# Performance work log

Measured on AMD Instinct MI355X. Metric: run time of the kernel, lower is better.

Reference implementation:

```python
import jax, jax.numpy as jnp
import numpy as np

B, DIM, N = 4, 256, 2048
HEADS, DIM_HEAD = 8, 64
HIDDEN = HEADS * DIM_HEAD
SCALE = DIM_HEAD ** -0.5


def setup_inputs() -> dict:
    key = jax.random.key(0)
    k0, k1, k2, k3 = jax.random.split(key, 4)
    x = jax.random.normal(k0, (B, DIM, N), dtype=jnp.float32)
    # Conv1d kernel-size-1 weights == plain matrices over channels
    w_qkv = jax.random.normal(k1, (3 * HIDDEN, DIM), dtype=jnp.float32) * (DIM ** -0.5)
    w_out = jax.random.normal(k2, (DIM, HIDDEN), dtype=jnp.float32) * (HIDDEN ** -0.5)
    b_out = jax.random.normal(k3, (DIM,), dtype=jnp.float32) * 0.01
    return {"x": x, "w_qkv": w_qkv, "w_out": w_out, "b_out": b_out}


def reference(x, w_qkv, w_out, b_out):
    b, c, n = x.shape
    # 1x1 conv projection: [3H, C] x [b, C, n] -> [b, 3H, n]
    qkv = jnp.einsum('oc,bcn->bon', w_qkv, x)
    q, k, v = jnp.split(qkv, 3, axis=1)
    # [b, heads, dim_head, n]
    q = q.reshape(b, HEADS, DIM_HEAD, n) * SCALE
    k = k.reshape(b, HEADS, DIM_HEAD, n)
    v = v.reshape(b, HEADS, DIM_HEAD, n)
    sim = jnp.einsum('bhcn,bhcm->bhnm', q, k)          # [b,h,n,n]
    attn = jax.nn.softmax(sim, axis=-1)
    out = jnp.einsum('bhnm,bhcm->bhcn', attn, v)       # [b,h,dh,n]
    out = out.reshape(b, HIDDEN, n)
    return jnp.einsum('oc,bcn->bon', w_out, out) + b_out[None, :, None]
```

## Files before the change

kernel.cpp:

```cpp
#include <hip/hip_runtime.h>
#include <math.h>

#define BB 4
#define CDIM 256
#define NN 2048
#define HEADS 8
#define DH 64
#define HIDDEN 512
#define THREEH 1536
#define QSCALE 0.18033688011112042f

typedef __attribute__((ext_vector_type(8))) short bf16x8;
typedef __attribute__((ext_vector_type(4))) float f32x4;

static __device__ inline unsigned short f2bf(float f) {
    unsigned u = __float_as_uint(f);
    u += 0x7fff + ((u >> 16) & 1);
    return (unsigned short)(u >> 16);
}
#if __has_builtin(__builtin_amdgcn_cvt_pk_bf16_f32)
static __device__ inline unsigned pk2(float a, float b) {
    auto v = __builtin_amdgcn_cvt_pk_bf16_f32(a, b);
    return __builtin_bit_cast(unsigned, v);
}
#else
static __device__ inline unsigned pk2(float a, float b) {
    return (unsigned)f2bf(a) | ((unsigned)f2bf(b) << 16);
}
#endif
#if __has_builtin(__builtin_amdgcn_exp2f)
#define EXP2(x) __builtin_amdgcn_exp2f(x)
#else
#define EXP2(x) exp2f(x)
#endif
#define MFMA16(a, b, c) __builtin_amdgcn_mfma_f32_16x16x32_bf16(a, b, c, 0, 0, 0)
#define SWZC(row, ch) ((((ch) ^ ((row) & 7)) << 3))

__global__ __launch_bounds__(256) void prep_w(const float* __restrict__ wqkv,
                                              const float* __restrict__ wout,
                                              unsigned* __restrict__ Wqb,
                                              unsigned* __restrict__ Wob) {
    const int t = blockIdx.x * 256 + threadIdx.x;
    if (t < 98304) {
        const int e = t * 4;
        const int o = e >> 8;
        const float s = (o < HIDDEN) ? QSCALE : 1.f;
        float4 v = *(const float4*)&wqkv[e];
        Wqb[t * 2 + 0] = pk2(v.x * s, v.y * s);
        Wqb[t * 2 + 1] = pk2(v.z * s, v.w * s);
    } else {
        const int e = (t - 98304) * 4;
        float4 v = *(const float4*)&wout[e];
        Wob[(t - 98304) * 2 + 0] = pk2(v.x, v.y);
        Wob[(t - 98304) * 2 + 1] = pk2(v.z, v.w);
    }
}

__global__ __launch_bounds__(256) void prep_x(const float* __restrict__ x,
                                              unsigned short* __restrict__ Xt) {
    __shared__ float Ls[64][65];
    const int n0 = blockIdx.x * 64, c0 = blockIdx.y * 64, b = blockIdx.z;
    const int t = threadIdx.x;
    const int r16 = t >> 4, c16 = t & 15;
#pragma unroll
    for (int s = 0; s < 4; ++s) {
        const int c = s * 16 + r16;
        float4 v = *(const float4*)&x[((size_t)(b * CDIM + c0 + c)) * NN + n0 + c16 * 4];
        *(float4*)&Ls[c][c16 * 4] = v;
    }
    __syncthreads();
#pragma unroll
    for (int s = 0; s < 4; ++s) {
        const int n = s * 16 + r16;
        const int c4 = c16 * 4;
        uint2 u;
        u.x = pk2(Ls[c4][n], Ls[c4 + 1][n]);
        u.y = pk2(Ls[c4 + 2][n], Ls[c4 + 3][n]);
        *(uint2*)&Xt[((size_t)(b * NN) + n0 + n) * CDIM + c0 + c4] = u;
    }
}

__global__ __launch_bounds__(256, 3) void qkv_gemm(const unsigned short* __restrict__ Xt,
                                                   const unsigned short* __restrict__ Wqb,
                                                   unsigned short* __restrict__ Qb,
                                                   unsigned short* __restrict__ Kb,
                                                   unsigned short* __restrict__ Vb) {
    __shared__ unsigned short Xs[128 * 64], Ws[128 * 64];
    const int bn0 = blockIdx.x * 128, o0 = blockIdx.y * 128;
    const int t = threadIdx.x, l = t & 63, w = t >> 6, lo = l & 15, quad = l >> 4;
    const int wo = (w >> 1) * 64, wn = (w & 1) * 64;
    const int sr = t >> 1, scb = (t & 1) * 4;
    const bool isV = (o0 >= 2 * HIDDEN);
    f32x4 acc[4][4];
#pragma unroll
    for (int i = 0; i < 4; ++i)
#pragma unroll
        for (int j = 0; j < 4; ++j) acc[i][j] = (f32x4){0.f, 0.f, 0.f, 0.f};

    for (int kc = 0; kc < CDIM; kc += 64) {
        __syncthreads();
#pragma unroll
        for (int j = 0; j < 4; ++j) {
            const int ch = scb + j;
            *(uint4*)&Xs[sr * 64 + SWZC(sr, ch)] =
                *(const uint4*)&Xt[(size_t)(bn0 + sr) * CDIM + kc + ch * 8];
            *(uint4*)&Ws[sr * 64 + SWZC(sr, ch)] =
                *(const uint4*)&Wqb[(size_t)(o0 + sr) * CDIM + kc + ch * 8];
        }
        __syncthreads();
#pragma unroll
        for (int kk = 0; kk < 2; ++kk) {
            const int swz = SWZC(lo, kk * 4 + quad);
            if (!isV) {
                bf16x8 af[4], bv[4];
#pragma unroll
                for (int ot = 0; ot < 4; ++ot) af[ot] = *(const bf16x8*)&Ws[(wo + ot * 16 + lo) * 64 + swz];
#pragma unroll
                for (int nt = 0; nt < 4; ++nt) bv[nt] = *(const bf16x8*)&Xs[(wn + nt * 16 + lo) * 64 + swz];
#pragma unroll
                for (int ot = 0; ot < 4; ++ot)
#pragma unroll
                    for (int nt = 0; nt < 4; ++nt) acc[ot][nt] = MFMA16(af[ot], bv[nt], acc[ot][nt]);
            } else {
                bf16x8 af[4], bv[4];
#pragma unroll
                for (int mt = 0; mt < 4; ++mt) af[mt] = *(const bf16x8*)&Xs[(wn + mt * 16 + lo) * 64 + swz];
#pragma unroll
                for (int ot = 0; ot < 4; ++ot) bv[ot] = *(const bf16x8*)&Ws[(wo + ot * 16 + lo) * 64 + swz];
#pragma unroll
                for (int mt = 0; mt < 4; ++mt)
#pragma unroll
                    for (int ot = 0; ot < 4; ++ot) acc[mt][ot] = MFMA16(af[mt], bv[ot], acc[mt][ot]);
            }
        }
    }
    if (!isV) {
#pragma unroll
        for (int ot = 0; ot < 4; ++ot) {
            const int og = o0 + wo + ot * 16 + quad * 4;
            const int h = (og >> 6) & 7;
            const int c0 = og & 63;
            unsigned short* dst = (og >= HIDDEN) ? Kb : Qb;
#pragma unroll
            for (int nt = 0; nt < 4; ++nt) {
                const int bn = bn0 + wn + nt * 16 + lo;
                const int b = bn >> 11, n = bn & 2047;
                uint2 u;
                u.x = pk2(acc[ot][nt][0], acc[ot][nt][1]);
                u.y = pk2(acc[ot][nt][2], acc[ot][nt][3]);
                *(uint2*)&dst[(((size_t)(b * HEADS + h)) * NN + n) * DH + c0] = u;
            }
        }
    } else {
#pragma unroll
        for (int mt = 0; mt < 4; ++mt) {
            const int bn = bn0 + wn + mt * 16 + quad * 4;
            const int b = bn >> 11, m = bn & 2047;
#pragma unroll
            for (int ot = 0; ot < 4; ++ot) {
                const int og = o0 + wo + ot * 16 + lo;
                const int h = (og >> 6) & 7;
                const int c = og & 63;
                uint2 u;
                u.x = pk2(acc[mt][ot][0], acc[mt][ot][1]);
                u.y = pk2(acc[mt][ot][2], acc[mt][ot][3]);
                *(uint2*)&Vb[(((size_t)(b * HEADS + h)) * DH + c) * NN + m] = u;
            }
        }
    }
}

__global__ __launch_bounds__(256, 6) void flash_attn(const unsigned short* __restrict__ Qb,
                                                     const unsigned short* __restrict__ Kb,
                                                     const unsigned short* __restrict__ Vb,
                                                     unsigned short* __restrict__ Yb) {
    __shared__ unsigned short Ks[64 * 64], Vs[64 * 64], Ps[64 * 64];
    const int flat = blockIdx.x;
    const int rest = flat >> 3;
    const int bh = ((rest & 3) << 3) | (flat & 7);
    const int q0 = (rest >> 2) * 64;
    const int b = bh >> 3, h = bh & 7;
    const int t = threadIdx.x, l = t & 63, w = t >> 6, lo = l & 15, quad = l >> 4;
    const unsigned short* Qp = Qb + (size_t)bh * NN * DH;
    const unsigned short* Kp = Kb + (size_t)bh * NN * DH;
    const unsigned short* Vp = Vb + (size_t)bh * DH * NN;
    const int q = q0 + 16 * w + lo;
    const bf16x8 bQ0 = *(const bf16x8*)&Qp[(size_t)q * DH + quad * 8];
    const bf16x8 bQ1 = *(const bf16x8*)&Qp[(size_t)q * DH + 32 + quad * 8];
    f32x4 O[4];
#pragma unroll
    for (int i = 0; i < 4; ++i) O[i] = (f32x4){0.f, 0.f, 0.f, 0.f};
    float m_i = -INFINITY, l_i = 0.f;
    const int sr = t >> 3, sc = t & 7;
    const int kst0 = sr * 64 + SWZC(sr, sc);
    const int key = lo & 7;

    for (int m0 = 0; m0 < NN; m0 += 64) {
        __syncthreads();
        *(uint4*)&Ks[kst0]           = *(const uint4*)&Kp[(size_t)(m0 + sr) * DH + sc * 8];
        *(uint4*)&Ks[kst0 + 32 * 64] = *(const uint4*)&Kp[(size_t)(m0 + sr + 32) * DH + sc * 8];
        *(uint4*)&Vs[kst0]           = *(const uint4*)&Vp[(size_t)sr * NN + m0 + sc * 8];
        *(uint4*)&Vs[kst0 + 32 * 64] = *(const uint4*)&Vp[(size_t)(sr + 32) * NN + m0 + sc * 8];
        __syncthreads();
        f32x4 S[4];
#pragma unroll
        for (int nt = 0; nt < 4; ++nt) {
            const int rb = (nt * 16 + lo) * 64;
            bf16x8 a0 = *(const bf16x8*)&Ks[rb + SWZC(lo, quad)];
            bf16x8 a1 = *(const bf16x8*)&Ks[rb + SWZC(lo, quad + 4)];
            f32x4 z = (f32x4){0.f, 0.f, 0.f, 0.f};
            z = MFMA16(a0, bQ0, z);
            z = MFMA16(a1, bQ1, z);
            S[nt] = z;
        }
        float mx;
        {
            f32x4 mm;
#pragma unroll
            for (int i = 0; i < 4; ++i)
                mm[i] = fmaxf(fmaxf(S[0][i], S[1][i]), fmaxf(S[2][i], S[3][i]));
            mx = fmaxf(fmaxf(mm[0], mm[1]), fmaxf(mm[2], mm[3]));
        }
        mx = fmaxf(mx, __shfl_xor(mx, 16));
        mx = fmaxf(mx, __shfl_xor(mx, 32));
        const float mn = fmaxf(m_i, mx);
        const float alpha = EXP2(m_i - mn);
        m_i = mn;
        float ls = 0.f;
        const int prow = (16 * w + lo) * 64;
#pragma unroll
        for (int nt = 0; nt < 4; ++nt) {
            f32x4 p;
#pragma unroll
            for (int i = 0; i < 4; ++i) p[i] = EXP2(S[nt][i] - mn);
            ls += (p[0] + p[1]) + (p[2] + p[3]);
            uint2 u;
            u.x = pk2(p[0], p[1]);
            u.y = pk2(p[2], p[3]);
            *(uint2*)&Ps[prow + (((nt * 2 + (quad >> 1)) ^ key) << 3) + (quad & 1) * 4] = u;
        }
        ls += __shfl_xor(ls, 16);
        ls += __shfl_xor(ls, 32);
        l_i = l_i * alpha + ls;
        asm volatile("s_waitcnt lgkmcnt(0)" ::: "memory");
#pragma unroll
        for (int ct = 0; ct < 4; ++ct) O[ct] *= alpha;
        const bf16x8 pb0 = *(const bf16x8*)&Ps[prow + SWZC(lo, quad)];
        const bf16x8 pb1 = *(const bf16x8*)&Ps[prow + SWZC(lo, quad + 4)];
#pragma unroll
        for (int ct = 0; ct < 4; ++ct) {
            const int rb = (ct * 16 + lo) * 64;
            bf16x8 a0 = *(const bf16x8*)&Vs[rb + SWZC(lo, quad)];
            bf16x8 a1 = *(const bf16x8*)&Vs[rb + SWZC(lo, quad + 4)];
            O[ct] = MFMA16(a0, pb0, O[ct]);
            O[ct] = MFMA16(a1, pb1, O[ct]);
        }
    }
    const float inv = 1.f / l_i;
    unsigned short* yrow = Yb + (((size_t)(b * NN) + q)) * HIDDEN + h * DH;
#pragma unroll
    for (int ct = 0; ct < 4; ++ct) {
        uint2 u;
        u.x = pk2(O[ct][0] * inv, O[ct][1] * inv);
        u.y = pk2(O[ct][2] * inv, O[ct][3] * inv);
        *(uint2*)&yrow[ct * 16 + quad * 4] = u;
    }
}

__global__ __launch_bounds__(256, 4) void out_gemm(const unsigned short* __restrict__ Yb,
                                                   const unsigned short* __restrict__ Wob,
                                                   const float* __restrict__ bias,
                                                   float* __restrict__ out) {
    __shared__ unsigned short Ys[128 * 64], Wos[64 * 64];
    const int bn0 = blockIdx.x * 128, o0 = blockIdx.y * 64;
    const int t = threadIdx.x, l = t & 63, w = t >> 6, lo = l & 15, quad = l >> 4;
    const int wn = w * 32;
    const int sr = t >> 1, scb = (t & 1) * 4;
    const int sr2 = t >> 2, scb2 = (t & 3) * 2;
    f32x4 acc[2][4];
#pragma unroll
    for (int i = 0; i < 2; ++i)
#pragma unroll
        for (int j = 0; j < 4; ++j) acc[i][j] = (f32x4){0.f, 0.f, 0.f, 0.f};

    for (int kc = 0; kc < HIDDEN; kc += 64) {
        __syncthreads();
#pragma unroll
        for (int j = 0; j < 4; ++j) {
            const int ch = scb + j;
            *(uint4*)&Ys[sr * 64 + SWZC(sr, ch)] =
                *(const uint4*)&Yb[(size_t)(bn0 + sr) * HIDDEN + kc + ch * 8];
        }
#pragma unroll
        for (int j = 0; j < 2; ++j) {
            const int ch = scb2 + j;
            *(uint4*)&Wos[sr2 * 64 + SWZC(sr2, ch)] =
                *(const uint4*)&Wob[(size_t)(o0 + sr2) * HIDDEN + kc + ch * 8];
        }
        __syncthreads();
#pragma unroll
        for (int kk = 0; kk < 2; ++kk) {
            const int swz = SWZC(lo, kk * 4 + quad);
            bf16x8 bv[4];
#pragma unroll
            for (int ot = 0; ot < 4; ++ot) bv[ot] = *(const bf16x8*)&Wos[(ot * 16 + lo) * 64 + swz];
#pragma unroll
            for (int mt = 0; mt < 2; ++mt) {
                bf16x8 av = *(const bf16x8*)&Ys[(wn + mt * 16 + lo) * 64 + swz];
#pragma unroll
                for (int ot = 0; ot < 4; ++ot) acc[mt][ot] = MFMA16(av, bv[ot], acc[mt][ot]);
            }
        }
    }
#pragma unroll
    for (int mt = 0; mt < 2; ++mt) {
        const int bn = bn0 + wn + mt * 16 + quad * 4;
        const int b = bn >> 11, n = bn & 2047;
#pragma unroll
        for (int ot = 0; ot < 4; ++ot) {
            const int o = o0 + ot * 16 + lo;
            *(f32x4*)&out[((size_t)(b * CDIM + o)) * NN + n] = acc[mt][ot] + bias[o];
        }
    }
}

extern "C" void kernel_launch(void* const* d_in, const int* in_sizes, int n_in,
                              void* d_out, int out_size, void* d_ws, size_t ws_size,
                              hipStream_t stream) {
    const float* x     = (const float*)d_in[0];
    const float* w_qkv = (const float*)d_in[1];
    const float* w_out = (const float*)d_in[2];
    const float* b_out = (const float*)d_in[3];
    float* out = (float*)d_out;

    unsigned short* Wqb = (unsigned short*)d_ws;
    unsigned short* Wob = Wqb + (size_t)THREEH * CDIM;
    unsigned short* Xt  = Wob + (size_t)CDIM * HIDDEN;
    unsigned short* Qb  = Xt + (size_t)BB * NN * CDIM;
    unsigned short* Kb  = Qb + (size_t)BB * HEADS * NN * DH;
    unsigned short* Vb  = Kb + (size_t)BB * HEADS * NN * DH;
    unsigned short* Yb  = Vb + (size_t)BB * HEADS * DH * NN;

    prep_w<<<512, 256, 0, stream>>>(w_qkv, w_out, (unsigned*)Wqb, (unsigned*)Wob);
    prep_x<<<dim3(NN / 64, CDIM / 64, BB), 256, 0, stream>>>(x, Xt);
    qkv_gemm<<<dim3(BB * NN / 128, THREEH / 128), 256, 0, stream>>>(Xt, Wqb, Qb, Kb, Vb);
    flash_attn<<<1024, 256, 0, stream>>>(Qb, Kb, Vb, Yb);
    out_gemm<<<dim3(BB * NN / 128, CDIM / 64), 256, 0, stream>>>(Yb, Wob, b_out, out);
}
```

Before: 164.7 us.

## Merge prep kernels and widen flash-attention tile to 128 queries with register prefetch

Merges the two preprocessing kernels into one launch, removing a kernel launch. In flash attention, each wave now handles 32 queries, so every K/V tile loaded into shared memory serves twice as many MFMAs. The next K/V tile is prefetched into registers to overlap global loads with compute. The row sum is computed with a ones-vector MFMA instead of shuffles, and O is rescaled only when a row max changes. In exchange the kernel uses more registers, its occupancy hint drops to 4, and the grid is halved to 512 blocks.

```diff
diff --git a/kernel.cpp b/kernel.cpp
--- a/kernel.cpp
+++ b/kernel.cpp
@@ -36,47 +36,55 @@
 #define MFMA16(a, b, c) __builtin_amdgcn_mfma_f32_16x16x32_bf16(a, b, c, 0, 0, 0)
 #define SWZC(row, ch) ((((ch) ^ ((row) & 7)) << 3))
 
-__global__ __launch_bounds__(256) void prep_w(const float* __restrict__ wqkv,
-                                              const float* __restrict__ wout,
-                                              unsigned* __restrict__ Wqb,
-                                              unsigned* __restrict__ Wob) {
-    const int t = blockIdx.x * 256 + threadIdx.x;
-    if (t < 98304) {
-        const int e = t * 4;
-        const int o = e >> 8;
-        const float s = (o < HIDDEN) ? QSCALE : 1.f;
-        float4 v = *(const float4*)&wqkv[e];
-        Wqb[t * 2 + 0] = pk2(v.x * s, v.y * s);
-        Wqb[t * 2 + 1] = pk2(v.z * s, v.w * s);
+__global__ __launch_bounds__(256) void prep_all(const float* __restrict__ x,
+                                                const float* __restrict__ wqkv,
+                                                const float* __restrict__ wout,
+                                                unsigned short* __restrict__ Xt,
+                                                unsigned* __restrict__ Wqb,
+                                                unsigned* __restrict__ Wob) {
+    __shared__ float Ls[64][65];
+    const int bx = blockIdx.x;
+    if (bx < 512) {
+        const int n0 = (bx & 31) * 64, c0 = ((bx >> 5) & 3) * 64, b = bx >> 7;
+        const int t = threadIdx.x;
+        const int r16 = t >> 4, c16 = t & 15;
+#pragma unroll
+        for (int s = 0; s < 4; ++s) {
+            const int c = s * 16 + r16;
+            float4 v = *(const float4*)&x[((size_t)(b * CDIM + c0 + c)) * NN + n0 + c16 * 4];
+            *(float4*)&Ls[c][c16 * 4] = v;
+        }
+        __syncthreads();
+#pragma unroll
+        for (int s = 0; s < 4; ++s) {
+            const int n = s * 16 + r16;
+            const int c4 = c16 * 4;
+            uint2 u;
+            u.x = pk2(Ls[c4][n], Ls[c4 + 1][n]);
+            u.y = pk2(Ls[c4 + 2][n], Ls[c4 + 3][n]);
+            *(uint2*)&Xt[((size_t)(b * NN) + n0 + n) * CDIM + c0 + c4] = u;
+        }
+    } else if (bx < 536) {
+        const int tt = (bx - 512) * 256 + threadIdx.x;
+#pragma unroll 4
+        for (int j = 0; j < 16; ++j) {
+            const int i4 = tt + j * 6144;
+            const int e = i4 * 4;
+            const float s = ((e >> 8) < HIDDEN) ? QSCALE : 1.f;
+            float4 v = *(const float4*)&wqkv[e];
+            Wqb[i4 * 2 + 0] = pk2(v.x * s, v.y * s);
+            Wqb[i4 * 2 + 1] = pk2(v.z * s, v.w * s);
+        }
     } else {
-        const int e = (t - 98304) * 4;
-        float4 v = *(const float4*)&wout[e];
-        Wob[(t - 98304) * 2 + 0] = pk2(v.x, v.y);
-        Wob[(t - 98304) * 2 + 1] = pk2(v.z, v.w);
-    }
-}
-
-__global__ __launch_bounds__(256) void prep_x(const float* __restrict__ x,
-                                              unsigned short* __restrict__ Xt) {
-    __shared__ float Ls[64][65];
-    const int n0 = blockIdx.x * 64, c0 = blockIdx.y * 64, b = blockIdx.z;
-    const int t = threadIdx.x;
-    const int r16 = t >> 4, c16 = t & 15;
-#pragma unroll
-    for (int s = 0; s < 4; ++s) {
-        const int c = s * 16 + r16;
-        float4 v = *(const float4*)&x[((size_t)(b * CDIM + c0 + c)) * NN + n0 + c16 * 4];
-        *(float4*)&Ls[c][c16 * 4] = v;
-    }
-    __syncthreads();
-#pragma unroll
-    for (int s = 0; s < 4; ++s) {
-        const int n = s * 16 + r16;
-        const int c4 = c16 * 4;
-        uint2 u;
-        u.x = pk2(Ls[c4][n], Ls[c4 + 1][n]);
-        u.y = pk2(Ls[c4 + 2][n], Ls[c4 + 3][n]);
-        *(uint2*)&Xt[((size_t)(b * NN) + n0 + n) * CDIM + c0 + c4] = u;
+        const int tt = (bx - 536) * 256 + threadIdx.x;
+#pragma unroll 4
+        for (int j = 0; j < 16; ++j) {
+            const int i4 = tt + j * 2048;
+            const int e = i4 * 4;
+            float4 v = *(const float4*)&wout[e];
+            Wob[i4 * 2 + 0] = pk2(v.x, v.y);
+            Wob[i4 * 2 + 1] = pk2(v.z, v.w);
+        }
     }
 }
 
@@ -170,100 +178,150 @@
     }
 }
 
-__global__ __launch_bounds__(256, 6) void flash_attn(const unsigned short* __restrict__ Qb,
+__global__ __launch_bounds__(256, 4) void flash_attn(const unsigned short* __restrict__ Qb,
                                                      const unsigned short* __restrict__ Kb,
                                                      const unsigned short* __restrict__ Vb,
                                                      unsigned short* __restrict__ Yb) {
-    __shared__ unsigned short Ks[64 * 64], Vs[64 * 64], Ps[64 * 64];
+    __shared__ unsigned short Ks[64 * 64], Vs[64 * 64], Ps[128 * 64];
     const int flat = blockIdx.x;
     const int rest = flat >> 3;
     const int bh = ((rest & 3) << 3) | (flat & 7);
-    const int q0 = (rest >> 2) * 64;
+    const int q0 = (rest >> 2) * 128;
     const int b = bh >> 3, h = bh & 7;
     const int t = threadIdx.x, l = t & 63, w = t >> 6, lo = l & 15, quad = l >> 4;
     const unsigned short* Qp = Qb + (size_t)bh * NN * DH;
     const unsigned short* Kp = Kb + (size_t)bh * NN * DH;
     const unsigned short* Vp = Vb + (size_t)bh * DH * NN;
-    const int q = q0 + 16 * w + lo;
-    const bf16x8 bQ0 = *(const bf16x8*)&Qp[(size_t)q * DH + quad * 8];
-    const bf16x8 bQ1 = *(const bf16x8*)&Qp[(size_t)q * DH + 32 + quad * 8];
-    f32x4 O[4];
-#pragma unroll
-    for (int i = 0; i < 4; ++i) O[i] = (f32x4){0.f, 0.f, 0.f, 0.f};
-    float m_i = -INFINITY, l_i = 0.f;
+    const int qbase = q0 + 32 * w;
+    bf16x8 bQ[2][2];
+#pragma unroll
+    for (int qt = 0; qt < 2; ++qt)
+#pragma unroll
+        for (int hh = 0; hh < 2; ++hh)
+            bQ[qt][hh] = *(const bf16x8*)&Qp[(size_t)(qbase + qt * 16 + lo) * DH + hh * 32 + quad * 8];
+    f32x4 O[4][2], lacc[2];
+#pragma unroll
+    for (int i = 0; i < 4; ++i)
+#pragma unroll
+        for (int j = 0; j < 2; ++j) O[i][j] = (f32x4){0.f, 0.f, 0.f, 0.f};
+#pragma unroll
+    for (int j = 0; j < 2; ++j) lacc[j] = (f32x4){0.f, 0.f, 0.f, 0.f};
+    float m_i[2] = {-INFINITY, -INFINITY};
     const int sr = t >> 3, sc = t & 7;
     const int kst0 = sr * 64 + SWZC(sr, sc);
     const int key = lo & 7;
-
+    const short oneb = (short)0x3F80;
+    bf16x8 aOnes;
+    {
+        const short v = (lo == 0) ? oneb : (short)0;
+        aOnes = (bf16x8){v, v, v, v, v, v, v, v};
+    }
+    uint4 rk0 = *(const uint4*)&Kp[(size_t)sr * DH + sc * 8];
+    uint4 rk1 = *(const uint4*)&Kp[(size_t)(sr + 32) * DH + sc * 8];
+    uint4 rv0 = *(const uint4*)&Vp[(size_t)sr * NN + sc * 8];
+    uint4 rv1 = *(const uint4*)&Vp[(size_t)(sr + 32) * NN + sc * 8];
+
+#pragma unroll 1
     for (int m0 = 0; m0 < NN; m0 += 64) {
         __syncthreads();
-        *(uint4*)&Ks[kst0]           = *(const uint4*)&Kp[(size_t)(m0 + sr) * DH + sc * 8];
-        *(uint4*)&Ks[kst0 + 32 * 64] = *(const uint4*)&Kp[(size_t)(m0 + sr + 32) * DH + sc * 8];
-        *(uint4*)&Vs[kst0]           = *(const uint4*)&Vp[(size_t)sr * NN + m0 + sc * 8];
-        *(uint4*)&Vs[kst0 + 32 * 64] = *(const uint4*)&Vp[(size_t)(sr + 32) * NN + m0 + sc * 8];
-        __syncthreads();
-        f32x4 S[4];
+        *(uint4*)&Ks[kst0] = rk0;
+        *(uint4*)&Ks[kst0 + 2048] = rk1;
+        *(uint4*)&Vs[kst0] = rv0;
+        *(uint4*)&Vs[kst0 + 2048] = rv1;
+        __syncthreads();
+        {
+            const int m1 = (m0 + 64 < NN) ? (m0 + 64) : m0;
+            rk0 = *(const uint4*)&Kp[(size_t)(m1 + sr) * DH + sc * 8];
+            rk1 = *(const uint4*)&Kp[(size_t)(m1 + sr + 32) * DH + sc * 8];
+            rv0 = *(const uint4*)&Vp[(size_t)sr * NN + m1 + sc * 8];
+            rv1 = *(const uint4*)&Vp[(size_t)(sr + 32) * NN + m1 + sc * 8];
+        }
+        f32x4 S[4][2];
 #pragma unroll
         for (int nt = 0; nt < 4; ++nt) {
             const int rb = (nt * 16 + lo) * 64;
             bf16x8 a0 = *(const bf16x8*)&Ks[rb + SWZC(lo, quad)];
             bf16x8 a1 = *(const bf16x8*)&Ks[rb + SWZC(lo, quad + 4)];
-            f32x4 z = (f32x4){0.f, 0.f, 0.f, 0.f};
-            z = MFMA16(a0, bQ0, z);
-            z = MFMA16(a1, bQ1, z);
-            S[nt] = z;
-        }
-        float mx;
-        {
+#pragma unroll
+            for (int qt = 0; qt < 2; ++qt) {
+                f32x4 z = (f32x4){0.f, 0.f, 0.f, 0.f};
+                z = MFMA16(a0, bQ[qt][0], z);
+                z = MFMA16(a1, bQ[qt][1], z);
+                S[nt][qt] = z;
+            }
+        }
+        float alpha[2];
+#pragma unroll
+        for (int qt = 0; qt < 2; ++qt) {
             f32x4 mm;
 #pragma unroll
             for (int i = 0; i < 4; ++i)
-                mm[i] = fmaxf(fmaxf(S[0][i], S[1][i]), fmaxf(S[2][i], S[3][i]));
-            mx = fmaxf(fmaxf(mm[0], mm[1]), fmaxf(mm[2], mm[3]));
-        }
-        mx = fmaxf(mx, __shfl_xor(mx, 16));
-        mx = fmaxf(mx, __shfl_xor(mx, 32));
-        const float mn = fmaxf(m_i, mx);
-        const float alpha = EXP2(m_i - mn);
-        m_i = mn;
-        float ls = 0.f;
-        const int prow = (16 * w + lo) * 64;
-#pragma unroll
-        for (int nt = 0; nt < 4; ++nt) {
-            f32x4 p;
-#pragma unroll
-            for (int i = 0; i < 4; ++i) p[i] = EXP2(S[nt][i] - mn);
-            ls += (p[0] + p[1]) + (p[2] + p[3]);
-            uint2 u;
-            u.x = pk2(p[0], p[1]);
-            u.y = pk2(p[2], p[3]);
-            *(uint2*)&Ps[prow + (((nt * 2 + (quad >> 1)) ^ key) << 3) + (quad & 1) * 4] = u;
-        }
-        ls += __shfl_xor(ls, 16);
-        ls += __shfl_xor(ls, 32);
-        l_i = l_i * alpha + ls;
+                mm[i] = fmaxf(fmaxf(S[0][qt][i], S[1][qt][i]), fmaxf(S[2][qt][i], S[3][qt][i]));
+            float mx = fmaxf(fmaxf(mm[0], mm[1]), fmaxf(mm[2], mm[3]));
+            mx = fmaxf(mx, __shfl_xor(mx, 16));
+            mx = fmaxf(mx, __shfl_xor(mx, 32));
+            const float mn = fmaxf(m_i[qt], mx);
+            alpha[qt] = EXP2(m_i[qt] - mn);
+            m_i[qt] = mn;
+            const int prow = (32 * w + qt * 16 + lo) * 64;
+#pragma unroll
+            for (int nt = 0; nt < 4; ++nt) {
+                f32x4 p;
+#pragma unroll
+                for (int i = 0; i < 4; ++i) p[i] = EXP2(S[nt][qt][i] - mn);
+                uint2 u;
+                u.x = pk2(p[0], p[1]);
+                u.y = pk2(p[2], p[3]);
+                *(uint2*)&Ps[prow + (((nt * 2 + (quad >> 1)) ^ key) << 3) + (quad & 1) * 4] = u;
+            }
+        }
         asm volatile("s_waitcnt lgkmcnt(0)" ::: "memory");
-#pragma unroll
-        for (int ct = 0; ct < 4; ++ct) O[ct] *= alpha;
-        const bf16x8 pb0 = *(const bf16x8*)&Ps[prow + SWZC(lo, quad)];
-        const bf16x8 pb1 = *(const bf16x8*)&Ps[prow + SWZC(lo, quad + 4)];
+        const float am = fminf(alpha[0], alpha[1]);
+        if (__ballot(am < 1.f)) {
+#pragma unroll
+            for (int qt = 0; qt < 2; ++qt) {
+#pragma unroll
+                for (int ct = 0; ct < 4; ++ct) O[ct][qt] *= alpha[qt];
+                lacc[qt] *= alpha[qt];
+            }
+        }
+        bf16x8 pb[2][2];
+#pragma unroll
+        for (int qt = 0; qt < 2; ++qt) {
+            const int prow = (32 * w + qt * 16 + lo) * 64;
+            pb[qt][0] = *(const bf16x8*)&Ps[prow + SWZC(lo, quad)];
+            pb[qt][1] = *(const bf16x8*)&Ps[prow + SWZC(lo, quad + 4)];
+        }
 #pragma unroll
         for (int ct = 0; ct < 4; ++ct) {
             const int rb = (ct * 16 + lo) * 64;
             bf16x8 a0 = *(const bf16x8*)&Vs[rb + SWZC(lo, quad)];
             bf16x8 a1 = *(const bf16x8*)&Vs[rb + SWZC(lo, quad + 4)];
-            O[ct] = MFMA16(a0, pb0, O[ct]);
-            O[ct] = MFMA16(a1, pb1, O[ct]);
-        }
-    }
-    const float inv = 1.f / l_i;
-    unsigned short* yrow = Yb + (((size_t)(b * NN) + q)) * HIDDEN + h * DH;
-#pragma unroll
-    for (int ct = 0; ct < 4; ++ct) {
-        uint2 u;
-        u.x = pk2(O[ct][0] * inv, O[ct][1] * inv);
-        u.y = pk2(O[ct][2] * inv, O[ct][3] * inv);
-        *(uint2*)&yrow[ct * 16 + quad * 4] = u;
+#pragma unroll
+            for (int qt = 0; qt < 2; ++qt) {
+                O[ct][qt] = MFMA16(a0, pb[qt][0], O[ct][qt]);
+                O[ct][qt] = MFMA16(a1, pb[qt][1], O[ct][qt]);
+            }
+        }
+#pragma unroll
+        for (int qt = 0; qt < 2; ++qt) {
+            lacc[qt] = MFMA16(aOnes, pb[qt][0], lacc[qt]);
+            lacc[qt] = MFMA16(aOnes, pb[qt][1], lacc[qt]);
+        }
+    }
+#pragma unroll
+    for (int qt = 0; qt < 2; ++qt) {
+        const float lv = __shfl(lacc[qt][0], lo);
+        const float inv = 1.f / lv;
+        const int q = qbase + qt * 16 + lo;
+        unsigned short* yrow = Yb + ((size_t)(b * NN) + q) * HIDDEN + h * DH;
+#pragma unroll
+        for (int ct = 0; ct < 4; ++ct) {
+            uint2 u;
+            u.x = pk2(O[ct][qt][0] * inv, O[ct][qt][1] * inv);
+            u.y = pk2(O[ct][qt][2] * inv, O[ct][qt][3] * inv);
+            *(uint2*)&yrow[ct * 16 + quad * 4] = u;
+        }
     }
 }
 
@@ -341,9 +399,8 @@
     unsigned short* Vb  = Kb + (size_t)BB * HEADS * NN * DH;
     unsigned short* Yb  = Vb + (size_t)BB * HEADS * DH * NN;
 
-    prep_w<<<512, 256, 0, stream>>>(w_qkv, w_out, (unsigned*)Wqb, (unsigned*)Wob);
-    prep_x<<<dim3(NN / 64, CDIM / 64, BB), 256, 0, stream>>>(x, Xt);
+    prep_all<<<544, 256, 0, stream>>>(x, w_qkv, w_out, Xt, (unsigned*)Wqb, (unsigned*)Wob);
     qkv_gemm<<<dim3(BB * NN / 128, THREEH / 128), 256, 0, stream>>>(Xt, Wqb, Qb, Kb, Vb);
-    flash_attn<<<1024, 256, 0, stream>>>(Qb, Kb, Vb, Yb);
+    flash_attn<<<512, 256, 0, stream>>>(Qb, Kb, Vb, Yb);
     out_gemm<<<dim3(BB * NN / 128, CDIM / 64), 256, 0, stream>>>(Yb, Wob, b_out, out);
 }
```

New measurement: 198.8 us. 1.21x slower.
